# Optimization experiments

Hardware: AMD Instinct MI355X
Metric: run time of the kernel (lower is better)

## Reference

```python
import jax, jax.numpy as jnp
import numpy as np

L = 7
D = 20
V = 2 ** L                      # voxel_size
NUM_EMB = V ** 3
DOM_LO, DOM_HI = -1.0, 1.0
DOM_LEN = DOM_HI - DOM_LO

# 8 corner offsets in the order used by the torch module
OFFSETS = jnp.array([[0, 0, 0], [1, 0, 0], [0, 1, 0], [1, 1, 0],
                     [0, 0, 1], [1, 0, 1], [0, 1, 1], [1, 1, 1]], dtype=jnp.int32)


def setup_inputs() -> dict:
    key = jax.random.key(0)
    kx, kg = jax.random.split(key)
    # points strictly inside the domain so floor()+1 corner stays in-range
    x = jax.random.uniform(kx, (1_000_000, 3), jnp.float32, minval=-1.0, maxval=0.998)
    grid = jax.random.normal(kg, (NUM_EMB, D), jnp.float32) * 0.02  # embedding table
    return {"x": x, "grid": grid}


def reference(x, grid):
    # points -> grid space, floor to lower corner
    gp = jnp.floor((x - DOM_LO) / DOM_LEN * V)                  # [P,3] float
    grid_idx = gp[:, None, :].astype(jnp.int32) + OFFSETS[None]  # [P,8,3]
    # flat index: ix * V^0 + iy * V^1 + iz * V^2
    flat = grid_idx[..., 0] + grid_idx[..., 1] * V + grid_idx[..., 2] * (V * V)
    Q_emb = grid[flat]                                          # [P,8,D] gather
    Q_pos = grid_idx.astype(x.dtype) / V * DOM_LEN + DOM_LO      # [P,8,3] world pos

    px, py, pz = x[:, 0], x[:, 1], x[:, 2]
    x1, x2 = Q_pos[:, 0, 0], Q_pos[:, 1, 0]
    y1, y2 = Q_pos[:, 0, 1], Q_pos[:, 2, 1]
    z1, z2 = Q_pos[:, 0, 2], Q_pos[:, 4, 2]

    q000, q100, q010, q110 = Q_emb[:, 0], Q_emb[:, 1], Q_emb[:, 2], Q_emb[:, 3]
    q001, q101, q011, q111 = Q_emb[:, 4], Q_emb[:, 5], Q_emb[:, 6], Q_emb[:, 7]

    wx0 = ((x2 - px) / (x2 - x1))[:, None]
    wx1 = ((px - x1) / (x2 - x1))[:, None]
    fx0 = wx0 * q000 + wx1 * q100
    fx1 = wx0 * q010 + wx1 * q110
    fx2 = wx0 * q001 + wx1 * q101
    fx3 = wx0 * q011 + wx1 * q111

    wy0 = ((y2 - py) / (y2 - y1))[:, None]
    wy1 = ((py - y1) / (y2 - y1))[:, None]
    fy0 = wy0 * fx0 + wy1 * fx1
    fy1 = wy0 * fx2 + wy1 * fx3

    wz0 = ((z2 - pz) / (z2 - z1))[:, None]
    wz1 = ((pz - z1) / (z2 - z1))[:, None]
    return wz0 * fy0 + wz1 * fy1                                 # [P,D]
```

## Files before the change

### kernel.cpp

```cpp
#include <hip/hip_runtime.h>

#define V 128
#define D 20
#define NUM_EMB (V * V * V)
#define NBUCK 4096
#define BCAP  512

typedef float v4f __attribute__((ext_vector_type(4)));
typedef unsigned int u32;

__device__ __forceinline__ void compute_chunk(
    const float* __restrict__ x, const float* __restrict__ grid,
    float* __restrict__ out, int i, int k)
{
    float px = x[3 * i + 0];
    float py = x[3 * i + 1];
    float pz = x[3 * i + 2];

    int ix = (int)floorf((px + 1.0f) * 64.0f);
    int iy = (int)floorf((py + 1.0f) * 64.0f);
    int iz = (int)floorf((pz + 1.0f) * 64.0f);

    float x1 = (float)ix * (2.0f / 128.0f) - 1.0f;
    float x2 = (float)(ix + 1) * (2.0f / 128.0f) - 1.0f;
    float y1 = (float)iy * (2.0f / 128.0f) - 1.0f;
    float y2 = (float)(iy + 1) * (2.0f / 128.0f) - 1.0f;
    float z1 = (float)iz * (2.0f / 128.0f) - 1.0f;
    float z2 = (float)(iz + 1) * (2.0f / 128.0f) - 1.0f;

    float wx1 = (px - x1) * 64.0f, wx0 = (x2 - px) * 64.0f;
    float wy1 = (py - y1) * 64.0f, wy0 = (y2 - py) * 64.0f;
    float wz1 = (pz - z1) * 64.0f, wz0 = (z2 - pz) * 64.0f;

    int f000 = ix + iy * V + iz * V * V;

    int flats[8];
    flats[0] = f000;
    flats[1] = f000 + 1;
    flats[2] = f000 + V;
    flats[3] = f000 + V + 1;
    flats[4] = f000 + V * V;
    flats[5] = f000 + V * V + 1;
    flats[6] = f000 + V * V + V;
    flats[7] = f000 + V * V + V + 1;

    #pragma unroll
    for (int c = 0; c < 8; c++) {
        if (flats[c] > NUM_EMB - 1) flats[c] = NUM_EMB - 1;
    }

    float w[8];
    w[0] = wx0 * wy0 * wz0;
    w[1] = wx1 * wy0 * wz0;
    w[2] = wx0 * wy1 * wz0;
    w[3] = wx1 * wy1 * wz0;
    w[4] = wx0 * wy0 * wz1;
    w[5] = wx1 * wy0 * wz1;
    w[6] = wx0 * wy1 * wz1;
    w[7] = wx1 * wy1 * wz1;

    v4f q[8];
    #pragma unroll
    for (int c = 0; c < 8; c++) {
        q[c] = *(const v4f*)(grid + (size_t)flats[c] * D + 4 * k);
    }

    v4f acc = (v4f)(0.0f);
    #pragma unroll
    for (int c = 0; c < 8; c++) {
        acc += w[c] * q[c];
    }

    __builtin_nontemporal_store(acc, (v4f*)(out + (size_t)i * D + 4 * k));
}

__global__ __launch_bounds__(256) void bin_kernel(
    const float* __restrict__ x, const float* __restrict__ grid,
    float* __restrict__ out, u32* __restrict__ cnt, u32* __restrict__ bucket,
    int N)
{
    int i = blockIdx.x * 256 + threadIdx.x;
    if (i >= N) return;
    float px = x[3 * i + 0];
    float py = x[3 * i + 1];
    float pz = x[3 * i + 2];
    int ix = (int)floorf((px + 1.0f) * 64.0f);
    int iy = (int)floorf((py + 1.0f) * 64.0f);
    int iz = (int)floorf((pz + 1.0f) * 64.0f);
    int b = (ix >> 3) + ((iy >> 3) << 4) + ((iz >> 3) << 8);
    u32 pos = atomicAdd(&cnt[b], 1u);
    if (pos < BCAP) {
        bucket[(size_t)b * BCAP + pos] = (u32)i;
    } else {
        for (int k = 0; k < 5; k++) compute_chunk(x, grid, out, i, k);
    }
}

__global__ __launch_bounds__(320) void gather_kernel(
    const float* __restrict__ x, const float* __restrict__ grid,
    float* __restrict__ out, const u32* __restrict__ cnt,
    const u32* __restrict__ bucket)
{
    int bid = blockIdx.x;
    int b = (bid & 7) * (NBUCK / 8) + (bid >> 3);

    u32 n = cnt[b];
    if (n > BCAP) n = BCAP;

    int tid = threadIdx.x;
    int lp  = tid / 5;
    int k   = tid - lp * 5;

    for (u32 base = 0; base < n; base += 64) {
        u32 p = base + (u32)lp;
        if (p < n) {
            int i = (int)bucket[(size_t)b * BCAP + p];
            compute_chunk(x, grid, out, i, k);
        }
    }
}

__global__ __launch_bounds__(320) void naive_kernel(
    const float* __restrict__ x, const float* __restrict__ grid,
    float* __restrict__ out, int N)
{
    int tid = threadIdx.x;
    int lp  = tid / 5;
    int k   = tid - lp * 5;
    int i   = blockIdx.x * 64 + lp;
    if (i >= N) return;
    compute_chunk(x, grid, out, i, k);
}

extern "C" void kernel_launch(void* const* d_in, const int* in_sizes, int n_in,
                              void* d_out, int out_size, void* d_ws, size_t ws_size,
                              hipStream_t stream) {
    const float* x = (const float*)d_in[0];
    const float* grid = (const float*)d_in[1];
    float* out = (float*)d_out;
    int N = in_sizes[0] / 3;

    size_t need = (size_t)NBUCK * 4 + (size_t)NBUCK * BCAP * 4;
    if (d_ws == nullptr || ws_size < need) {
        int nblocks = (N + 63) / 64;
        naive_kernel<<<nblocks, 320, 0, stream>>>(x, grid, out, N);
        return;
    }

    u32* cnt = (u32*)d_ws;
    u32* bucket = cnt + NBUCK;

    hipMemsetAsync(cnt, 0, (size_t)NBUCK * 4, stream);
    bin_kernel<<<(N + 255) / 256, 256, 0, stream>>>(x, grid, out, cnt, bucket, N);
    gather_kernel<<<NBUCK, 320, 0, stream>>>(x, grid, out, cnt, bucket);
}
```

Baseline: 416.0 us.

## Stage per-bucket grid region into LDS and interpolate from shared memory

Each gather block now copies its 9x9x9 neighbourhood of embedding rows into LDS with global_load_lds before interpolating. The 8 corner reads per point then come from shared memory instead of global memory, and the weights are computed directly from the fractional coordinates. Points that overflow a bucket are written to a separate list and handled by a small extra kernel instead of inline in the bin kernel. In exchange, every bucket pays the staging cost even when it holds few points, and the large LDS allocation (about 58 KB) limits occupancy.

```diff
diff --git a/kernel.cpp b/kernel.cpp
--- a/kernel.cpp
+++ b/kernel.cpp
@@ -5,9 +5,18 @@
 #define NUM_EMB (V * V * V)
 #define NBUCK 4096
 #define BCAP  512
+#define OVFCAP 4096
+#define REG_ROWS 729
+#define REG_CHUNKS 3645
+#define STAGE_INSTS 57
 
 typedef float v4f __attribute__((ext_vector_type(4)));
 typedef unsigned int u32;
+
+typedef const __attribute__((address_space(1))) void gv_t;
+typedef __attribute__((address_space(3))) void lv_t;
+#define G2L(gsrc, ldst) \
+    __builtin_amdgcn_global_load_lds((gv_t*)(gsrc), (lv_t*)(ldst), 16, 0, 0)
 
 __device__ __forceinline__ void compute_chunk(
     const float* __restrict__ x, const float* __restrict__ grid,
@@ -16,7 +25,6 @@
     float px = x[3 * i + 0];
     float py = x[3 * i + 1];
     float pz = x[3 * i + 2];
-
     int ix = (int)floorf((px + 1.0f) * 64.0f);
     int iy = (int)floorf((py + 1.0f) * 64.0f);
     int iz = (int)floorf((pz + 1.0f) * 64.0f);
@@ -33,51 +41,36 @@
     float wz1 = (pz - z1) * 64.0f, wz0 = (z2 - pz) * 64.0f;
 
     int f000 = ix + iy * V + iz * V * V;
-
-    int flats[8];
-    flats[0] = f000;
-    flats[1] = f000 + 1;
-    flats[2] = f000 + V;
-    flats[3] = f000 + V + 1;
-    flats[4] = f000 + V * V;
-    flats[5] = f000 + V * V + 1;
-    flats[6] = f000 + V * V + V;
-    flats[7] = f000 + V * V + V + 1;
-
+    int flats[8] = { f000,             f000 + 1,
+                     f000 + V,         f000 + V + 1,
+                     f000 + V * V,     f000 + V * V + 1,
+                     f000 + V * V + V, f000 + V * V + V + 1 };
     #pragma unroll
-    for (int c = 0; c < 8; c++) {
+    for (int c = 0; c < 8; c++)
         if (flats[c] > NUM_EMB - 1) flats[c] = NUM_EMB - 1;
-    }
 
     float w[8];
-    w[0] = wx0 * wy0 * wz0;
-    w[1] = wx1 * wy0 * wz0;
-    w[2] = wx0 * wy1 * wz0;
-    w[3] = wx1 * wy1 * wz0;
-    w[4] = wx0 * wy0 * wz1;
-    w[5] = wx1 * wy0 * wz1;
-    w[6] = wx0 * wy1 * wz1;
-    w[7] = wx1 * wy1 * wz1;
+    w[0] = wx0 * wy0 * wz0; w[1] = wx1 * wy0 * wz0;
+    w[2] = wx0 * wy1 * wz0; w[3] = wx1 * wy1 * wz0;
+    w[4] = wx0 * wy0 * wz1; w[5] = wx1 * wy0 * wz1;
+    w[6] = wx0 * wy1 * wz1; w[7] = wx1 * wy1 * wz1;
 
     v4f q[8];
     #pragma unroll
-    for (int c = 0; c < 8; c++) {
+    for (int c = 0; c < 8; c++)
         q[c] = *(const v4f*)(grid + (size_t)flats[c] * D + 4 * k);
-    }
 
     v4f acc = (v4f)(0.0f);
     #pragma unroll
-    for (int c = 0; c < 8; c++) {
-        acc += w[c] * q[c];
-    }
+    for (int c = 0; c < 8; c++) acc += w[c] * q[c];
 
     __builtin_nontemporal_store(acc, (v4f*)(out + (size_t)i * D + 4 * k));
 }
 
 __global__ __launch_bounds__(256) void bin_kernel(
     const float* __restrict__ x, const float* __restrict__ grid,
-    float* __restrict__ out, u32* __restrict__ cnt, u32* __restrict__ bucket,
-    int N)
+    float* __restrict__ out, u32* __restrict__ cnt, u32* __restrict__ blist,
+    u32* __restrict__ ovfc, u32* __restrict__ ovf, int N)
 {
     int i = blockIdx.x * 256 + threadIdx.x;
     if (i >= N) return;
@@ -90,33 +83,93 @@
     int b = (ix >> 3) + ((iy >> 3) << 4) + ((iz >> 3) << 8);
     u32 pos = atomicAdd(&cnt[b], 1u);
     if (pos < BCAP) {
-        bucket[(size_t)b * BCAP + pos] = (u32)i;
+        blist[(size_t)b * BCAP + pos] = (u32)i;
     } else {
-        for (int k = 0; k < 5; k++) compute_chunk(x, grid, out, i, k);
-    }
-}
-
-__global__ __launch_bounds__(320) void gather_kernel(
+        u32 op = atomicAdd(ovfc, 1u);
+        if (op < OVFCAP) ovf[op] = (u32)i;
+        else for (int k = 0; k < 5; k++) compute_chunk(x, grid, out, i, k);
+    }
+}
+
+__global__ __launch_bounds__(256) void gather_kernel(
     const float* __restrict__ x, const float* __restrict__ grid,
     float* __restrict__ out, const u32* __restrict__ cnt,
-    const u32* __restrict__ bucket)
-{
+    const u32* __restrict__ blist)
+{
+    __shared__ __align__(16) float reg[14640];
+
     int bid = blockIdx.x;
     int b = (bid & 7) * (NBUCK / 8) + (bid >> 3);
+    int bx = b & 15, by = (b >> 4) & 15, bz = b >> 8;
+    int gx0 = bx * 8, gy0 = by * 8, gz0 = bz * 8;
+
+    int tid = threadIdx.x, wave = tid >> 6, lane = tid & 63;
+
+    for (int w = wave; w < STAGE_INSTS; w += 4) {
+        int t = w * 64 + lane;
+        if (t > REG_CHUNKS - 1) t = REG_CHUNKS - 1;
+        int row = t / 5;
+        int c   = t - row * 5;
+        int sx = row % 9;
+        int r9 = row / 9;
+        int sy = r9 % 9;
+        int sz = r9 / 9;
+        int flat = (gx0 + sx) + (gy0 + sy) * V + (gz0 + sz) * (V * V);
+        if (flat > NUM_EMB - 1) flat = NUM_EMB - 1;
+        G2L(grid + (size_t)flat * D + c * 4, reg + w * 256);
+    }
+
+    __syncthreads();
 
     u32 n = cnt[b];
     if (n > BCAP) n = BCAP;
-
-    int tid = threadIdx.x;
-    int lp  = tid / 5;
-    int k   = tid - lp * 5;
-
-    for (u32 base = 0; base < n; base += 64) {
-        u32 p = base + (u32)lp;
-        if (p < n) {
-            int i = (int)bucket[(size_t)b * BCAP + p];
-            compute_chunk(x, grid, out, i, k);
+    int total = (int)n * 5;
+    for (int u = tid; u < total; u += 256) {
+        int p = u / 5;
+        int k = u - p * 5;
+        int i = (int)blist[(size_t)b * BCAP + p];
+        float px = x[3 * i + 0];
+        float py = x[3 * i + 1];
+        float pz = x[3 * i + 2];
+        float gxf = (px + 1.0f) * 64.0f;
+        float gyf = (py + 1.0f) * 64.0f;
+        float gzf = (pz + 1.0f) * 64.0f;
+        float ixf = floorf(gxf), iyf = floorf(gyf), izf = floorf(gzf);
+        float fx = gxf - ixf;
+        float fy = gyf - iyf;
+        float fz = gzf - izf;
+        int lx = (int)ixf - gx0;
+        int ly = (int)iyf - gy0;
+        int lz = (int)izf - gz0;
+        int l000 = (lz * 9 + ly) * 9 + lx;
+
+        v4f acc = (v4f)(0.0f);
+        #pragma unroll
+        for (int c = 0; c < 8; c++) {
+            int l = l000 + (c & 1) + ((c >> 1) & 1) * 9 + ((c >> 2) & 1) * 81;
+            v4f q = *(const v4f*)(reg + l * 20 + k * 4);
+            float wgt = ((c & 1)        ? fx : 1.0f - fx)
+                      * (((c >> 1) & 1) ? fy : 1.0f - fy)
+                      * (((c >> 2) & 1) ? fz : 1.0f - fz);
+            acc += wgt * q;
         }
+        __builtin_nontemporal_store(acc, (v4f*)(out + (size_t)i * D + k * 4));
+    }
+}
+
+__global__ __launch_bounds__(256) void ovf_kernel(
+    const float* __restrict__ x, const float* __restrict__ grid,
+    float* __restrict__ out, const u32* __restrict__ ovfc,
+    const u32* __restrict__ ovf)
+{
+    u32 n = *ovfc;
+    if (n > OVFCAP) n = OVFCAP;
+    int total = (int)n * 5;
+    for (int u = blockIdx.x * 256 + threadIdx.x; u < total;
+         u += 256 * (int)gridDim.x) {
+        int p = u / 5;
+        int k = u - p * 5;
+        compute_chunk(x, grid, out, (int)ovf[p], k);
     }
 }
 
@@ -140,17 +193,21 @@
     float* out = (float*)d_out;
     int N = in_sizes[0] / 3;
 
-    size_t need = (size_t)NBUCK * 4 + (size_t)NBUCK * BCAP * 4;
+    size_t need = ((size_t)NBUCK + 1 + OVFCAP + (size_t)NBUCK * BCAP) * 4;
     if (d_ws == nullptr || ws_size < need) {
         int nblocks = (N + 63) / 64;
         naive_kernel<<<nblocks, 320, 0, stream>>>(x, grid, out, N);
         return;
     }
 
-    u32* cnt = (u32*)d_ws;
-    u32* bucket = cnt + NBUCK;
-
-    hipMemsetAsync(cnt, 0, (size_t)NBUCK * 4, stream);
-    bin_kernel<<<(N + 255) / 256, 256, 0, stream>>>(x, grid, out, cnt, bucket, N);
-    gather_kernel<<<NBUCK, 320, 0, stream>>>(x, grid, out, cnt, bucket);
-}
+    u32* cnt   = (u32*)d_ws;
+    u32* ovfc  = cnt + NBUCK;
+    u32* ovf   = ovfc + 1;
+    u32* blist = ovf + OVFCAP;
+
+    hipMemsetAsync(cnt, 0, (size_t)(NBUCK + 1) * 4, stream);
+    bin_kernel<<<(N + 255) / 256, 256, 0, stream>>>(
+        x, grid, out, cnt, blist, ovfc, ovf, N);
+    gather_kernel<<<NBUCK, 256, 0, stream>>>(x, grid, out, cnt, blist);
+    ovf_kernel<<<16, 256, 0, stream>>>(x, grid, out, ovfc, ovf);
+}
```

Measured after the change: 395.8 us. 4.9% less time.
